# Optimization experiments

Measured on AMD Instinct MI355X. Metric: run time of the kernel, lower is better.

Reference implementation:

```python
import jax, jax.numpy as jnp
import numpy as np

LEVELS = [(128, 128), (64, 64), (32, 32), (16, 16)]  # (H_l, W_l) per feature level
N_TOTAL = sum(h * w for h, w in LEVELS)  # 21760
B, D, H, P, L = 2, 256, 8, 4, 4
HD = D // H
FFN_DIM = 1024


def setup_inputs() -> dict:
    key = jax.random.key(0)
    ks = jax.random.split(key, 12)
    s = 0.02  # weight init scale
    return {
        'embed': jax.random.normal(ks[0], (B, N_TOTAL, D), jnp.float32),
        'pos': jax.random.normal(ks[1], (B, N_TOTAL, D), jnp.float32),
        'ref_points': jax.random.uniform(ks[2], (B, N_TOTAL, L, 2), jnp.float32),
        'ln1_w': jnp.ones((D,), jnp.float32), 'ln1_b': jnp.zeros((D,), jnp.float32),
        'ln2_w': jnp.ones((D,), jnp.float32), 'ln2_b': jnp.zeros((D,), jnp.float32),
        'Wv': jax.random.normal(ks[3], (D, D), jnp.float32) * s, 'bv': jnp.zeros((D,), jnp.float32),
        'Woff': jax.random.normal(ks[4], (D, H * L * P * 2), jnp.float32) * s, 'boff': jnp.zeros((H * L * P * 2,), jnp.float32),
        'Wattn': jax.random.normal(ks[5], (D, H * L * P), jnp.float32) * s, 'battn': jnp.zeros((H * L * P,), jnp.float32),
        'Wo': jax.random.normal(ks[6], (D, D), jnp.float32) * s, 'bo': jnp.zeros((D,), jnp.float32),
        'W1': jax.random.normal(ks[7], (D, FFN_DIM), jnp.float32) * s, 'b1': jnp.zeros((FFN_DIM,), jnp.float32),
        'W2': jax.random.normal(ks[8], (FFN_DIM, D), jnp.float32) * s, 'b2': jnp.zeros((D,), jnp.float32),
        'dimensions': jnp.array(LEVELS, jnp.int32),
    }


def _layer_norm(x, w, b):
    m = jnp.mean(x, axis=-1, keepdims=True)
    v = jnp.mean(jnp.square(x - m), axis=-1, keepdims=True)
    return (x - m) * jax.lax.rsqrt(v + 1e-5) * w + b


def _msda(q, ref, v, dims, Wv, bv, Woff, boff, Wattn, battn, Wo, bo):
    # q, v: (B, N, D); ref: (B, N, L, 2) normalized (x, y)
    Bq, N, _ = q.shape
    value = (v @ Wv + bv).reshape(Bq, N, H, HD)
    off = (q @ Woff + boff).reshape(Bq, N, H, L, P, 2)
    aw = jax.nn.softmax((q @ Wattn + battn).reshape(Bq, N, H, L * P), axis=-1)
    aw = aw.reshape(Bq, N, H, L, P)
    # offset normalizer is [W_l, H_l]
    norm = jnp.stack([dims[:, 1], dims[:, 0]], axis=-1).astype(q.dtype)  # (L, 2)
    loc = ref[:, :, None, :, None, :] + off / norm[None, None, None, :, None, :]  # (B,N,H,L,P,2)

    out = jnp.zeros((Bq, N, H, HD), q.dtype)
    start = 0
    for l, (Hl, Wl) in enumerate(LEVELS):
        S = Hl * Wl
        vl = value[:, start:start + S].transpose(0, 2, 1, 3)  # (B, H, S, hd)
        start += S
        # grid_sample semantics: align_corners=False, zero padding
        x = loc[:, :, :, l, :, 0] * Wl - 0.5  # (B, N, H, P)
        y = loc[:, :, :, l, :, 1] * Hl - 0.5
        x0 = jnp.floor(x); y0 = jnp.floor(y)
        wx = x - x0; wy = y - y0
        x0i = x0.astype(jnp.int32); y0i = y0.astype(jnp.int32)
        samp = jnp.zeros(x.shape + (HD,), q.dtype)
        for dy, dx, w in ((0, 0, (1 - wx) * (1 - wy)), (0, 1, wx * (1 - wy)),
                          (1, 0, (1 - wx) * wy), (1, 1, wx * wy)):
            xi = x0i + dx; yi = y0i + dy
            valid = (xi >= 0) & (xi < Wl) & (yi >= 0) & (yi < Hl)
            idx = jnp.clip(yi, 0, Hl - 1) * Wl + jnp.clip(xi, 0, Wl - 1)  # (B, N, H, P)
            idx_t = idx.transpose(0, 2, 1, 3).reshape(Bq, H, N * P)
            g = jnp.take_along_axis(vl, idx_t[..., None], axis=2)  # (B, H, N*P, hd)
            g = g.reshape(Bq, H, N, P, HD).transpose(0, 2, 1, 3, 4)  # (B, N, H, P, hd)
            samp = samp + (w * valid)[..., None] * g
        out = out + jnp.sum(samp * aw[:, :, :, l, :, None], axis=3)
    return out.reshape(Bq, N, D) @ Wo + bo


def reference(embed, pos, ref_points, ln1_w, ln1_b, ln2_w, ln2_b, Wv, bv, Woff, boff,
              Wattn, battn, Wo, bo, W1, b1, W2, b2, dimensions):
    v = _layer_norm(embed, ln1_w, ln1_b)
    q = v + pos
    embed = embed + _msda(q, ref_points, v, dimensions, Wv, bv, Woff, boff, Wattn, battn, Wo, bo)
    f = _layer_norm(embed, ln2_w, ln2_b)
    embed = embed + jax.nn.relu(f @ W1 + b1) @ W2 + b2
    return embed
```

## Files before the change

kernel.cpp:

```cpp
#include <hip/hip_runtime.h>
#include <cstdint>
#include <cstddef>

#define N_TOTAL 21760
#define BATCH   2
#define M_TOT   (BATCH * N_TOTAL)
#define DMODEL  256
#define NHEAD   8
#define HDIM    32
#define FFN     1024

typedef __bf16 b16x8 __attribute__((ext_vector_type(8)));
typedef float  f32x4 __attribute__((ext_vector_type(4)));

typedef const __attribute__((address_space(1))) void g_void;
typedef __attribute__((address_space(3))) void lds_void;

__device__ __forceinline__ unsigned short f2b(float f) {
  union { float f; unsigned u; } v; v.f = f;
  unsigned r = v.u + 0x7FFF + ((v.u >> 16) & 1);
  return (unsigned short)(r >> 16);
}
__device__ __forceinline__ float b2f(unsigned short u) {
  union { unsigned u; float f; } v; v.u = (unsigned)u << 16;
  return v.f;
}

__device__ __forceinline__ int xcd_wgid(int bid, int nwg) {
  int q = nwg >> 3, r = nwg & 7;
  int xcd = bid & 7, k = bid >> 3;
  return (xcd < r ? xcd * (q + 1) : r * (q + 1) + (xcd - r) * q) + k;
}

__global__ void wconv_all(const float* __restrict__ Wv, const float* __restrict__ Woff,
                          const float* __restrict__ Wattn, const float* __restrict__ Wo,
                          const float* __restrict__ W1, const float* __restrict__ W2,
                          unsigned short* __restrict__ dstbase) {
  int idx = blockIdx.x * 256 + threadIdx.x;
  const float* src; int K, N, off;
  if (idx < 65536)       { src = Wv;    K = 256;  N = 256;  off = 0;      }
  else if (idx < 131072) { src = Woff;  K = 256;  N = 256;  off = 65536;  idx -= 65536; }
  else if (idx < 163840) { src = Wattn; K = 256;  N = 128;  off = 131072; idx -= 131072; }
  else if (idx < 229376) { src = Wo;    K = 256;  N = 256;  off = 163840; idx -= 163840; }
  else if (idx < 491520) { src = W1;    K = 256;  N = 1024; off = 229376; idx -= 229376; }
  else if (idx < 753664) { src = W2;    K = 1024; N = 256;  off = 491520; idx -= 491520; }
  else return;
  int k = idx / N, n = idx - k * N;
  dstbase[off + (size_t)n * K + k] = f2b(src[idx]);
}

__global__ void ln1_kernel(const float* __restrict__ x, const float* __restrict__ pos,
                           const float* __restrict__ w, const float* __restrict__ b,
                           unsigned short* __restrict__ vb, unsigned short* __restrict__ qb) {
  int t = threadIdx.x;
  int tkn = blockIdx.x * 4 + (t >> 6);
  int lane = t & 63;
  size_t base = (size_t)tkn * DMODEL + lane * 4;
  float4 xv = *(const float4*)&x[base];
  float s1 = xv.x + xv.y + xv.z + xv.w;
  float s2 = xv.x * xv.x + xv.y * xv.y + xv.z * xv.z + xv.w * xv.w;
  #pragma unroll
  for (int off = 32; off; off >>= 1) {
    s1 += __shfl_down(s1, off);
    s2 += __shfl_down(s2, off);
  }
  s1 = __shfl(s1, 0); s2 = __shfl(s2, 0);
  float m   = s1 * (1.0f / DMODEL);
  float var = s2 * (1.0f / DMODEL) - m * m;
  float rs  = rsqrtf(var + 1e-5f);
  float4 wv = *(const float4*)&w[lane * 4];
  float4 bv = *(const float4*)&b[lane * 4];
  float4 pv = *(const float4*)&pos[base];
  float o0 = (xv.x - m) * rs * wv.x + bv.x;
  float o1 = (xv.y - m) * rs * wv.y + bv.y;
  float o2 = (xv.z - m) * rs * wv.z + bv.z;
  float o3 = (xv.w - m) * rs * wv.w + bv.w;
  ushort4 vo = {f2b(o0), f2b(o1), f2b(o2), f2b(o3)};
  ushort4 qo = {f2b(o0 + pv.x), f2b(o1 + pv.y), f2b(o2 + pv.z), f2b(o3 + pv.w)};
  *(ushort4*)&vb[base] = vo;
  *(ushort4*)&qb[base] = qo;
}

__device__ __forceinline__ void gemm_core(
    const unsigned short* __restrict__ A, const unsigned short* __restrict__ Bt,
    const float* __restrict__ bias,
    const float* __restrict__ addf, const unsigned short* __restrict__ addb,
    float* __restrict__ Cf, unsigned short* __restrict__ Cb,
    int K, int N, int relu, int row0, int col0,
    unsigned short* S ) {
  unsigned short* As = S;
  unsigned short* Bs = S + 8192;
  int t  = threadIdx.x;
  int w  = t >> 6;
  int l  = t & 63;
  int wm = w >> 1, wn = w & 1;
  int lr = l & 15;
  int kq = l >> 4;

  f32x4 acc[4][4];
  #pragma unroll
  for (int i = 0; i < 4; ++i)
    #pragma unroll
    for (int j = 0; j < 4; ++j) acc[i][j] = (f32x4){0.f, 0.f, 0.f, 0.f};

  int srow = l >> 3;
  int swseg = ((l & 7) ^ srow) * 8;

  for (int k0 = 0; k0 < K; k0 += 64) {
    #pragma unroll
    for (int i = 0; i < 4; ++i) {
      int c = w * 4 + i;
      const unsigned short* ga = A  + (size_t)(row0 + c * 8 + srow) * K + k0 + swseg;
      const unsigned short* gb = Bt + (size_t)(col0 + c * 8 + srow) * K + k0 + swseg;
      __builtin_amdgcn_global_load_lds((g_void*)ga, (lds_void*)(As + c * 512), 16, 0, 0);
      __builtin_amdgcn_global_load_lds((g_void*)gb, (lds_void*)(Bs + c * 512), 16, 0, 0);
    }
    __syncthreads();
    #pragma unroll
    for (int kk = 0; kk < 2; ++kk) {
      b16x8 aF[4], bF[4];
      #pragma unroll
      for (int i = 0; i < 4; ++i) {
        int row = wm * 64 + i * 16 + lr;
        int gp = (kk * 4 + kq) ^ (lr & 7);
        aF[i] = *(const b16x8*)&As[row * 64 + gp * 8];
      }
      #pragma unroll
      for (int j = 0; j < 4; ++j) {
        int row = wn * 64 + j * 16 + lr;
        int gp = (kk * 4 + kq) ^ (lr & 7);
        bF[j] = *(const b16x8*)&Bs[row * 64 + gp * 8];
      }
      #pragma unroll
      for (int i = 0; i < 4; ++i)
        #pragma unroll
        for (int j = 0; j < 4; ++j)
          acc[i][j] = __builtin_amdgcn_mfma_f32_16x16x32_bf16(aF[i], bF[j], acc[i][j], 0, 0, 0);
    }
    __syncthreads();
  }

  if (Cb) {
    #pragma unroll
    for (int j = 0; j < 4; ++j) {
      int coll = wn * 64 + j * 16 + lr;
      int colg = col0 + coll;
      float bcol = bias[colg];
      #pragma unroll
      for (int i = 0; i < 4; ++i) {
        int rl0 = wm * 64 + i * 16 + kq * 4;
        #pragma unroll
        for (int r = 0; r < 4; ++r) {
          int rowl = rl0 + r;
          float o = acc[i][j][r] + bcol;
          if (relu) o = fmaxf(o, 0.0f);
          if (addf) o += addf[(size_t)(row0 + rowl) * N + colg];
          if (addb) o += b2f(addb[(size_t)(row0 + rowl) * N + colg]);
          S[rowl * 128 + (coll ^ ((rowl & 3) << 5))] = f2b(o);
        }
      }
    }
    __syncthreads();
    #pragma unroll
    for (int m = 0; m < 8; ++m) {
      int cc = m * 256 + t;
      int row = cc >> 4, g = cc & 15;
      float4 v = *(const float4*)&S[row * 128 + ((g ^ ((row & 3) << 2)) << 3)];
      *(float4*)&Cb[(size_t)(row0 + row) * N + col0 + g * 8] = v;
    }
  } else {
    #pragma unroll
    for (int j = 0; j < 4; ++j) {
      int colg = col0 + wn * 64 + j * 16 + lr;
      float bcol = bias[colg];
      #pragma unroll
      for (int i = 0; i < 4; ++i) {
        int r0g = row0 + wm * 64 + i * 16 + kq * 4;
        #pragma unroll
        for (int r = 0; r < 4; ++r) {
          int rowg = r0g + r;
          float o = acc[i][j][r] + bcol;
          if (relu) o = fmaxf(o, 0.0f);
          if (addf) o += addf[(size_t)rowg * N + colg];
          if (addb) o += b2f(addb[(size_t)rowg * N + colg]);
          Cf[(size_t)rowg * N + colg] = o;
        }
      }
    }
  }
}

__global__ __launch_bounds__(256, 3)
void gemm_bf16(const unsigned short* __restrict__ A,
               const unsigned short* __restrict__ Bt,
               const float* __restrict__ bias,
               const float* __restrict__ addf, const unsigned short* __restrict__ addb,
               float* __restrict__ Cf, unsigned short* __restrict__ Cb,
               int K, int N, int relu, int ncolt) {
  __shared__ unsigned short S[16384];
  int wgid = xcd_wgid(blockIdx.x, gridDim.x);
  int row0 = (wgid / ncolt) * 128;
  int col0 = (wgid % ncolt) * 128;
  gemm_core(A, Bt, bias, addf, addb, Cf, Cb, K, N, relu, row0, col0, S);
}

__global__ __launch_bounds__(256, 3)
void gemm_proj(const unsigned short* __restrict__ vb,
               const unsigned short* __restrict__ qb,
               const unsigned short* __restrict__ Wvt,
               const unsigned short* __restrict__ Wofft,
               const unsigned short* __restrict__ Wattnt,
               const float* __restrict__ bv, const float* __restrict__ boff,
               const float* __restrict__ battn,
               unsigned short* __restrict__ valb,
               unsigned short* __restrict__ offb,
               unsigned short* __restrict__ awb) {
  __shared__ unsigned short S[16384];
  int wgid = xcd_wgid(blockIdx.x, gridDim.x);
  int y = wgid % 5;
  int row0 = (wgid / 5) * 128;
  const unsigned short* A; const unsigned short* Bt; const float* bias;
  unsigned short* C; int col0, N;
  if (y < 2)      { A = vb; Bt = Wvt;    bias = bv;    C = valb; col0 = y * 128;       N = 256; }
  else if (y < 4) { A = qb; Bt = Wofft;  bias = boff;  C = offb; col0 = (y - 2) * 128; N = 256; }
  else            { A = qb; Bt = Wattnt; bias = battn; C = awb;  col0 = 0;             N = 128; }
  gemm_core(A, Bt, bias, nullptr, nullptr, nullptr, C, 256, N, 0, row0, col0, S);
}

__global__ __launch_bounds__(512, 2)
void gemm_wo_ln2(const unsigned short* __restrict__ A,
                 const unsigned short* __restrict__ Bt,
                 const float* __restrict__ bias,
                 const float* __restrict__ emb,
                 const float* __restrict__ lnw, const float* __restrict__ lnb,
                 unsigned short* __restrict__ emb2b,
                 unsigned short* __restrict__ fb16) {
  __shared__ unsigned short S[24576];
  __shared__ float lnS1[128 * 4], lnS2[128 * 4];
  __shared__ float lnM[128], lnR[128];
  unsigned short* As = S;
  unsigned short* Bs = S + 8192;
  int t  = threadIdx.x;
  int w  = t >> 6;
  int l  = t & 63;
  int wm = w >> 2, wn = w & 3;
  int lr = l & 15;
  int kq = l >> 4;
  int row0 = xcd_wgid(blockIdx.x, gridDim.x) * 128;

  f32x4 acc[4][4];
  #pragma unroll
  for (int i = 0; i < 4; ++i)
    #pragma unroll
    for (int j = 0; j < 4; ++j) acc[i][j] = (f32x4){0.f, 0.f, 0.f, 0.f};

  int srow = l >> 3;
  int swseg = ((l & 7) ^ srow) * 8;

  for (int k0 = 0; k0 < 256; k0 += 64) {
    #pragma unroll
    for (int i = 0; i < 2; ++i) {
      int c = w * 2 + i;
      const unsigned short* ga = A + (size_t)(row0 + c * 8 + srow) * 256 + k0 + swseg;
      __builtin_amdgcn_global_load_lds((g_void*)ga, (lds_void*)(As + c * 512), 16, 0, 0);
    }
    #pragma unroll
    for (int i = 0; i < 4; ++i) {
      int c = w * 4 + i;
      const unsigned short* gb = Bt + (size_t)(c * 8 + srow) * 256 + k0 + swseg;
      __builtin_amdgcn_global_load_lds((g_void*)gb, (lds_void*)(Bs + c * 512), 16, 0, 0);
    }
    __syncthreads();
    #pragma unroll
    for (int kk = 0; kk < 2; ++kk) {
      b16x8 aF[4], bF[4];
      #pragma unroll
      for (int i = 0; i < 4; ++i) {
        int row = wm * 64 + i * 16 + lr;
        int gp = (kk * 4 + kq) ^ (lr & 7);
        aF[i] = *(const b16x8*)&As[row * 64 + gp * 8];
      }
      #pragma unroll
      for (int j = 0; j < 4; ++j) {
        int row = wn * 64 + j * 16 + lr;
        int gp = (kk * 4 + kq) ^ (lr & 7);
        bF[j] = *(const b16x8*)&Bs[row * 64 + gp * 8];
      }
      #pragma unroll
      for (int i = 0; i < 4; ++i)
        #pragma unroll
        for (int j = 0; j < 4; ++j)
          acc[i][j] = __builtin_amdgcn_mfma_f32_16x16x32_bf16(aF[i], bF[j], acc[i][j], 0, 0, 0);
    }
    __syncthreads();
  }

  float s1[4][4] = {}, s2[4][4] = {};
  #pragma unroll
  for (int j = 0; j < 4; ++j) {
    int colg = wn * 64 + j * 16 + lr;
    float bcol = bias[colg];
    #pragma unroll
    for (int i = 0; i < 4; ++i) {
      int rowg = row0 + wm * 64 + i * 16 + kq * 4;
      #pragma unroll
      for (int r = 0; r < 4; ++r) {
        float o = acc[i][j][r] + bcol + emb[(size_t)(rowg + r) * 256 + colg];
        acc[i][j][r] = o;
        s1[i][r] += o;
        s2[i][r] += o * o;
      }
    }
  }
  #pragma unroll
  for (int m = 1; m < 16; m <<= 1) {
    #pragma unroll
    for (int i = 0; i < 4; ++i)
      #pragma unroll
      for (int r = 0; r < 4; ++r) {
        s1[i][r] += __shfl_xor(s1[i][r], m);
        s2[i][r] += __shfl_xor(s2[i][r], m);
      }
  }
  if (lr == 0) {
    #pragma unroll
    for (int i = 0; i < 4; ++i)
      #pragma unroll
      for (int r = 0; r < 4; ++r) {
        int rl = wm * 64 + i * 16 + kq * 4 + r;
        lnS1[rl * 4 + wn] = s1[i][r];
        lnS2[rl * 4 + wn] = s2[i][r];
      }
  }
  __syncthreads();
  if (t < 128) {
    float a = lnS1[t * 4] + lnS1[t * 4 + 1] + lnS1[t * 4 + 2] + lnS1[t * 4 + 3];
    float b = lnS2[t * 4] + lnS2[t * 4 + 1] + lnS2[t * 4 + 2] + lnS2[t * 4 + 3];
    float m = a * (1.0f / 256.0f);
    float var = b * (1.0f / 256.0f) - m * m;
    lnM[t] = m;
    lnR[t] = rsqrtf(var + 1e-5f);
  }
  __syncthreads();

  #pragma unroll
  for (int outn = 0; outn < 2; ++outn) {
    unsigned short* dst = outn == 0 ? emb2b : fb16;
    #pragma unroll
    for (int half = 0; half < 2; ++half) {
      __syncthreads();
      if ((wn >> 1) == half) {
        #pragma unroll
        for (int j = 0; j < 4; ++j) {
          int colg = wn * 64 + j * 16 + lr;
          int coll = colg - half * 128;
          #pragma unroll
          for (int i = 0; i < 4; ++i) {
            #pragma unroll
            for (int r = 0; r < 4; ++r) {
              int rowl = wm * 64 + i * 16 + kq * 4 + r;
              float o = acc[i][j][r];
              float vv = outn == 0 ? o
                  : (o - lnM[rowl]) * lnR[rowl] * lnw[colg] + lnb[colg];
              S[rowl * 128 + (coll ^ ((rowl & 3) << 5))] = f2b(vv);
            }
          }
        }
      }
      __syncthreads();
      #pragma unroll
      for (int m = 0; m < 4; ++m) {
        int cc = m * 512 + t;
        int row = cc >> 4, g = cc & 15;
        float4 v = *(const float4*)&S[row * 128 + ((g ^ ((row & 3) << 2)) << 3)];
        *(float4*)&dst[(size_t)(row0 + row) * 256 + half * 128 + g * 8] = v;
      }
    }
  }
}

__global__ void msda_kernel(const unsigned short* __restrict__ value,
                            const unsigned short* __restrict__ offb,
                            const unsigned short* __restrict__ awb,
                            const float* __restrict__ ref,
                            unsigned short* __restrict__ outb) {
  __shared__ int2 P[544] __attribute__((aligned(16)));
  int bid = blockIdx.x;
  int tkn = (bid & 7) * (M_TOT / 8) + (bid >> 3);
  int t   = threadIdx.x;
  int b   = (tkn >= N_TOTAL) ? 1 : 0;

  if (t < 128) {
    int h = t >> 4, s = t & 15, lev = s >> 2, p = s & 3;
    float lg = b2f(awb[(size_t)tkn * 128 + h * 16 + s]);
    float mx = lg;
    #pragma unroll
    for (int m = 1; m < 16; m <<= 1) mx = fmaxf(mx, __shfl_xor(mx, m, 16));
    float e = __expf(lg - mx);
    float sum = e;
    #pragma unroll
    for (int m = 1; m < 16; m <<= 1) sum += __shfl_xor(sum, m, 16);
    float aw = e / sum;

    const int HL[4] = {128, 64, 32, 16};
    const int ST[4] = {0, 16384, 20480, 21504};
    int Wl = HL[lev];
    float rx = ref[(size_t)tkn * 8 + lev * 2 + 0];
    float ry = ref[(size_t)tkn * 8 + lev * 2 + 1];
    float ox = b2f(offb[(size_t)tkn * 256 + h * 32 + lev * 8 + p * 2 + 0]);
    float oy = b2f(offb[(size_t)tkn * 256 + h * 32 + lev * 8 + p * 2 + 1]);
    float x = rx * (float)Wl + ox - 0.5f;
    float y = ry * (float)Wl + oy - 0.5f;
    float x0f = floorf(x), y0f = floorf(y);
    float wx = x - x0f, wy = y - y0f;
    int x0 = (int)x0f, y0 = (int)y0f;
    float wt[4] = {(1.f - wx) * (1.f - wy), wx * (1.f - wy),
                   (1.f - wx) * wy, wx * wy};
    int base = b * N_TOTAL + ST[lev];
    #pragma unroll
    for (int tp = 0; tp < 4; ++tp) {
      int e4 = s * 4 + tp;
      int idx = h * 68 + (e4 >> 5) * 34 + (e4 & 31);
      int xi = x0 + (tp & 1), yi = y0 + (tp >> 1);
      bool ok = (xi >= 0) & (xi < Wl) & (yi >= 0) & (yi < Wl);
      float wgt = ok ? aw * wt[tp] : 0.f;
      int boff2 = ok ? (((base + yi * Wl + xi) * 256 + h * 32) * 2) : 0;
      P[idx] = (int2){__float_as_int(wgt), boff2};
    }
  }
  __syncthreads();

  int h = t >> 5, g = t & 31, dp = g & 15, half = g >> 4;
  int o = h * 68 + half * 34;
  unsigned doff = dp * 4;
  const char* vbase = (const char*)value;
  float accL = 0.f, accH = 0.f;
  #pragma unroll 4
  for (int j2 = 0; j2 < 16; ++j2) {
    int4 pr2 = *(const int4*)&P[o + j2 * 2];
    float wgt0 = __int_as_float(pr2.x);
    float wgt1 = __int_as_float(pr2.z);
    unsigned v0 = *(const unsigned*)(vbase + (size_t)((unsigned)pr2.y + doff));
    unsigned v1 = *(const unsigned*)(vbase + (size_t)((unsigned)pr2.w + doff));
    union { unsigned u; float f; } l0, h0, l1, h1;
    l0.u = v0 << 16; h0.u = v0 & 0xffff0000u;
    l1.u = v1 << 16; h1.u = v1 & 0xffff0000u;
    accL += wgt0 * l0.f + wgt1 * l1.f;
    accH += wgt0 * h0.f + wgt1 * h1.f;
  }
  accL += __shfl_xor(accL, 16);
  accH += __shfl_xor(accH, 16);
  if (half == 0) {
    unsigned pk = (unsigned)f2b(accL) | ((unsigned)f2b(accH) << 16);
    *(unsigned*)&outb[(size_t)tkn * 256 + h * 32 + dp * 2] = pk;
  }
}

extern "C" void kernel_launch(void* const* d_in, const int* in_sizes, int n_in,
                              void* d_out, int out_size, void* d_ws, size_t ws_size,
                              hipStream_t stream) {
  const float* embed = (const float*)d_in[0];
  const float* pos   = (const float*)d_in[1];
  const float* refp  = (const float*)d_in[2];
  const float* ln1w  = (const float*)d_in[3];
  const float* ln1b  = (const float*)d_in[4];
  const float* ln2w  = (const float*)d_in[5];
  const float* ln2b  = (const float*)d_in[6];
  const float* Wv    = (const float*)d_in[7];
  const float* bv    = (const float*)d_in[8];
  const float* Woff  = (const float*)d_in[9];
  const float* boff  = (const float*)d_in[10];
  const float* Wattn = (const float*)d_in[11];
  const float* battn = (const float*)d_in[12];
  const float* Wo    = (const float*)d_in[13];
  const float* bo    = (const float*)d_in[14];
  const float* W1    = (const float*)d_in[15];
  const float* b1    = (const float*)d_in[16];
  const float* W2    = (const float*)d_in[17];
  const float* b2    = (const float*)d_in[18];
  float* out = (float*)d_out;
  float* ws  = (float*)d_ws;

  const size_t U = (size_t)M_TOT * DMODEL;
  unsigned short* valb16 = (unsigned short*)ws;
  unsigned short* offb16 = (unsigned short*)(ws + U / 2);
  unsigned short* awb16  = (unsigned short*)(ws + U);
  unsigned short* msdab  = (unsigned short*)(ws + U + U / 4);
  unsigned short* hid16  = (unsigned short*)ws;
  unsigned short* emb2b  = (unsigned short*)(ws + 2 * U);
  unsigned short* vb16   = (unsigned short*)(ws + 3 * U);
  unsigned short* qb16   = (unsigned short*)(ws + 3 * U + U / 2);
  unsigned short* fb16   = (unsigned short*)(ws + 4 * U);
  unsigned short* wbuf   = (unsigned short*)(ws + 4 * U + U / 2);

  unsigned short* Wvt    = wbuf;
  unsigned short* Wofft  = wbuf + 65536;
  unsigned short* Wattnt = wbuf + 131072;
  unsigned short* Wot    = wbuf + 163840;
  unsigned short* W1t    = wbuf + 229376;
  unsigned short* W2t    = wbuf + 491520;

  wconv_all<<<(753664 + 255) / 256, 256, 0, stream>>>(Wv, Woff, Wattn, Wo, W1, W2, wbuf);

  ln1_kernel<<<M_TOT / 4, 256, 0, stream>>>(embed, pos, ln1w, ln1b, vb16, qb16);

  gemm_proj<<<(M_TOT / 128) * 5, 256, 0, stream>>>(
      vb16, qb16, Wvt, Wofft, Wattnt, bv, boff, battn, valb16, offb16, awb16);

  msda_kernel<<<M_TOT, 256, 0, stream>>>(valb16, offb16, awb16, refp, msdab);

  gemm_wo_ln2<<<M_TOT / 128, 512, 0, stream>>>(
      msdab, Wot, bo, embed, ln2w, ln2b, emb2b, fb16);

  gemm_bf16<<<(M_TOT / 128) * 8, 256, 0, stream>>>(
      fb16, W1t, b1, nullptr, nullptr, nullptr, hid16, 256, 1024, 1, 8);
  gemm_bf16<<<(M_TOT / 128) * 2, 256, 0, stream>>>(
      hid16, W2t, b2, nullptr, emb2b, out, nullptr, 1024, 256, 0, 2);
}
```

Baseline: 293.7 us.

## Double-buffer LDS tiles in GEMM kernels and use packed FMA in MSDA gather

Splits the GEMM K-loop into a prefetch stage that loads the next K-tile into a second LDS buffer while MFMAs run on the current one. This removes one of the two barriers per iteration and overlaps global-to-LDS loads with compute. LDS use doubles, and launch bounds drop from 3 to 2 blocks per CU, which lowers occupancy. The MSDA gather loop is also rewritten to process one sample per iteration with a 2-wide float vector accumulate, aiming for packed FMA. It drops the 16-byte LDS alignment on P.

Measured after the change: 311.5 us. +6.1%, slower.

```diff
diff --git a/kernel.cpp b/kernel.cpp
--- a/kernel.cpp
+++ b/kernel.cpp
@@ -12,6 +12,7 @@
 
 typedef __bf16 b16x8 __attribute__((ext_vector_type(8)));
 typedef float  f32x4 __attribute__((ext_vector_type(4)));
+typedef float  f32x2 __attribute__((ext_vector_type(2)));
 
 typedef const __attribute__((address_space(1))) void g_void;
 typedef __attribute__((address_space(3))) void lds_void;
@@ -87,9 +88,7 @@
     const float* __restrict__ addf, const unsigned short* __restrict__ addb,
     float* __restrict__ Cf, unsigned short* __restrict__ Cb,
     int K, int N, int relu, int row0, int col0,
-    unsigned short* S ) {
-  unsigned short* As = S;
-  unsigned short* Bs = S + 8192;
+    unsigned short* S) {
   int t  = threadIdx.x;
   int w  = t >> 6;
   int l  = t & 63;
@@ -106,7 +105,7 @@
   int srow = l >> 3;
   int swseg = ((l & 7) ^ srow) * 8;
 
-  for (int k0 = 0; k0 < K; k0 += 64) {
+  auto stage = [&](unsigned short* As, unsigned short* Bs, int k0) {
     #pragma unroll
     for (int i = 0; i < 4; ++i) {
       int c = w * 4 + i;
@@ -115,7 +114,16 @@
       __builtin_amdgcn_global_load_lds((g_void*)ga, (lds_void*)(As + c * 512), 16, 0, 0);
       __builtin_amdgcn_global_load_lds((g_void*)gb, (lds_void*)(Bs + c * 512), 16, 0, 0);
     }
-    __syncthreads();
+  };
+
+  unsigned short* Ac = S;         unsigned short* Bc = S + 8192;
+  unsigned short* An = S + 16384; unsigned short* Bn = S + 24576;
+
+  stage(Ac, Bc, 0);
+  __syncthreads();
+
+  for (int k0 = 0; k0 < K; k0 += 64) {
+    if (k0 + 64 < K) stage(An, Bn, k0 + 64);
     #pragma unroll
     for (int kk = 0; kk < 2; ++kk) {
       b16x8 aF[4], bF[4];
@@ -123,13 +131,13 @@
       for (int i = 0; i < 4; ++i) {
         int row = wm * 64 + i * 16 + lr;
         int gp = (kk * 4 + kq) ^ (lr & 7);
-        aF[i] = *(const b16x8*)&As[row * 64 + gp * 8];
+        aF[i] = *(const b16x8*)&Ac[row * 64 + gp * 8];
       }
       #pragma unroll
       for (int j = 0; j < 4; ++j) {
         int row = wn * 64 + j * 16 + lr;
         int gp = (kk * 4 + kq) ^ (lr & 7);
-        bF[j] = *(const b16x8*)&Bs[row * 64 + gp * 8];
+        bF[j] = *(const b16x8*)&Bc[row * 64 + gp * 8];
       }
       #pragma unroll
       for (int i = 0; i < 4; ++i)
@@ -138,6 +146,8 @@
           acc[i][j] = __builtin_amdgcn_mfma_f32_16x16x32_bf16(aF[i], bF[j], acc[i][j], 0, 0, 0);
     }
     __syncthreads();
+    unsigned short* tA = Ac; Ac = An; An = tA;
+    unsigned short* tB = Bc; Bc = Bn; Bn = tB;
   }
 
   if (Cb) {
@@ -190,21 +200,21 @@
   }
 }
 
-__global__ __launch_bounds__(256, 3)
+__global__ __launch_bounds__(256, 2)
 void gemm_bf16(const unsigned short* __restrict__ A,
                const unsigned short* __restrict__ Bt,
                const float* __restrict__ bias,
                const float* __restrict__ addf, const unsigned short* __restrict__ addb,
                float* __restrict__ Cf, unsigned short* __restrict__ Cb,
                int K, int N, int relu, int ncolt) {
-  __shared__ unsigned short S[16384];
+  __shared__ unsigned short S[32768];
   int wgid = xcd_wgid(blockIdx.x, gridDim.x);
   int row0 = (wgid / ncolt) * 128;
   int col0 = (wgid % ncolt) * 128;
   gemm_core(A, Bt, bias, addf, addb, Cf, Cb, K, N, relu, row0, col0, S);
 }
 
-__global__ __launch_bounds__(256, 3)
+__global__ __launch_bounds__(256, 2)
 void gemm_proj(const unsigned short* __restrict__ vb,
                const unsigned short* __restrict__ qb,
                const unsigned short* __restrict__ Wvt,
@@ -215,7 +225,7 @@
                unsigned short* __restrict__ valb,
                unsigned short* __restrict__ offb,
                unsigned short* __restrict__ awb) {
-  __shared__ unsigned short S[16384];
+  __shared__ unsigned short S[32768];
   int wgid = xcd_wgid(blockIdx.x, gridDim.x);
   int y = wgid % 5;
   int row0 = (wgid / 5) * 128;
@@ -235,11 +245,9 @@
                  const float* __restrict__ lnw, const float* __restrict__ lnb,
                  unsigned short* __restrict__ emb2b,
                  unsigned short* __restrict__ fb16) {
-  __shared__ unsigned short S[24576];
+  __shared__ unsigned short S[49152];
   __shared__ float lnS1[128 * 4], lnS2[128 * 4];
   __shared__ float lnM[128], lnR[128];
-  unsigned short* As = S;
-  unsigned short* Bs = S + 8192;
   int t  = threadIdx.x;
   int w  = t >> 6;
   int l  = t & 63;
@@ -257,7 +265,7 @@
   int srow = l >> 3;
   int swseg = ((l & 7) ^ srow) * 8;
 
-  for (int k0 = 0; k0 < 256; k0 += 64) {
+  auto stage = [&](unsigned short* As, unsigned short* Bs, int k0) {
     #pragma unroll
     for (int i = 0; i < 2; ++i) {
       int c = w * 2 + i;
@@ -270,7 +278,16 @@
       const unsigned short* gb = Bt + (size_t)(c * 8 + srow) * 256 + k0 + swseg;
       __builtin_amdgcn_global_load_lds((g_void*)gb, (lds_void*)(Bs + c * 512), 16, 0, 0);
     }
-    __syncthreads();
+  };
+
+  unsigned short* Ac = S;         unsigned short* Bc = S + 8192;
+  unsigned short* An = S + 24576; unsigned short* Bn = S + 32768;
+
+  stage(Ac, Bc, 0);
+  __syncthreads();
+
+  for (int k0 = 0; k0 < 256; k0 += 64) {
+    if (k0 + 64 < 256) stage(An, Bn, k0 + 64);
     #pragma unroll
     for (int kk = 0; kk < 2; ++kk) {
       b16x8 aF[4], bF[4];
@@ -278,13 +295,13 @@
       for (int i = 0; i < 4; ++i) {
         int row = wm * 64 + i * 16 + lr;
         int gp = (kk * 4 + kq) ^ (lr & 7);
-        aF[i] = *(const b16x8*)&As[row * 64 + gp * 8];
+        aF[i] = *(const b16x8*)&Ac[row * 64 + gp * 8];
       }
       #pragma unroll
       for (int j = 0; j < 4; ++j) {
         int row = wn * 64 + j * 16 + lr;
         int gp = (kk * 4 + kq) ^ (lr & 7);
-        bF[j] = *(const b16x8*)&Bs[row * 64 + gp * 8];
+        bF[j] = *(const b16x8*)&Bc[row * 64 + gp * 8];
       }
       #pragma unroll
       for (int i = 0; i < 4; ++i)
@@ -293,6 +310,8 @@
           acc[i][j] = __builtin_amdgcn_mfma_f32_16x16x32_bf16(aF[i], bF[j], acc[i][j], 0, 0, 0);
     }
     __syncthreads();
+    unsigned short* tA = Ac; Ac = An; An = tA;
+    unsigned short* tB = Bc; Bc = Bn; Bn = tB;
   }
 
   float s1[4][4] = {}, s2[4][4] = {};
@@ -384,7 +403,7 @@
                             const unsigned short* __restrict__ awb,
                             const float* __restrict__ ref,
                             unsigned short* __restrict__ outb) {
-  __shared__ int2 P[544] __attribute__((aligned(16)));
+  __shared__ int2 P[544];
   int bid = blockIdx.x;
   int tkn = (bid & 7) * (M_TOT / 8) + (bid >> 3);
   int t   = threadIdx.x;
@@ -434,24 +453,23 @@
   int o = h * 68 + half * 34;
   unsigned doff = dp * 4;
   const char* vbase = (const char*)value;
-  float accL = 0.f, accH = 0.f;
-  #pragma unroll 4
-  for (int j2 = 0; j2 < 16; ++j2) {
-    int4 pr2 = *(const int4*)&P[o + j2 * 2];
-    float wgt0 = __int_as_float(pr2.x);
-    float wgt1 = __int_as_float(pr2.z);
-    unsigned v0 = *(const unsigned*)(vbase + (size_t)((unsigned)pr2.y + doff));
-    unsigned v1 = *(const unsigned*)(vbase + (size_t)((unsigned)pr2.w + doff));
-    union { unsigned u; float f; } l0, h0, l1, h1;
-    l0.u = v0 << 16; h0.u = v0 & 0xffff0000u;
-    l1.u = v1 << 16; h1.u = v1 & 0xffff0000u;
-    accL += wgt0 * l0.f + wgt1 * l1.f;
-    accH += wgt0 * h0.f + wgt1 * h1.f;
-  }
-  accL += __shfl_xor(accL, 16);
-  accH += __shfl_xor(accH, 16);
+  f32x2 acc = {0.f, 0.f};
+  #pragma unroll 8
+  for (int j = 0; j < 32; ++j) {
+    int2 pr = P[o + j];
+    float wgt = __int_as_float(pr.x);
+    unsigned v = *(const unsigned*)(vbase + (size_t)((unsigned)pr.y + doff));
+    union { unsigned u; float f; } lo, hi;
+    lo.u = v << 16;
+    hi.u = v & 0xffff0000u;
+    f32x2 vv = {lo.f, hi.f};
+    f32x2 w2 = {wgt, wgt};
+    acc += w2 * vv;
+  }
+  acc.x += __shfl_xor(acc.x, 16);
+  acc.y += __shfl_xor(acc.y, 16);
   if (half == 0) {
-    unsigned pk = (unsigned)f2b(accL) | ((unsigned)f2b(accH) << 16);
+    unsigned pk = (unsigned)f2b(acc.x) | ((unsigned)f2b(acc.y) << 16);
     *(unsigned*)&outb[(size_t)tkn * 256 + h * 32 + dp * 2] = pk;
   }
 }
```
